# Kernel optimization log

Hardware: AMD Instinct MI355X
Metric: run time of the kernel (lower is better)

Reference implementation:

```python
import jax, jax.numpy as jnp
import numpy as np

B, T, C = 2, 2048, 2048
N_HEAD = 16
N_KV = 4
HEAD = C // N_HEAD  # 128
GROUP = N_HEAD // N_KV


def setup_inputs() -> dict:
    key = jax.random.key(0)
    ks = jax.random.split(key, 5)
    s = 1.0 / np.sqrt(C)
    return {
        "x": jax.random.normal(ks[0], (B, T, C), dtype=jnp.float32),
        "Wq": jax.random.normal(ks[1], (C, C), dtype=jnp.float32) * s,
        "Wk": jax.random.normal(ks[2], (C, N_KV * HEAD), dtype=jnp.float32) * s,
        "Wv": jax.random.normal(ks[3], (C, N_KV * HEAD), dtype=jnp.float32) * s,
        "Wo": jax.random.normal(ks[4], (C, C), dtype=jnp.float32) * s,
    }


def reference(x, Wq, Wk, Wv, Wo):
    Bx, Tx, Cx = x.shape
    q = (x @ Wq).reshape(Bx, Tx, N_HEAD, HEAD).transpose(0, 2, 1, 3)  # (B,H,T,D)
    k = (x @ Wk).reshape(Bx, Tx, N_KV, HEAD).transpose(0, 2, 1, 3)    # (B,KV,T,D)
    v = (x @ Wv).reshape(Bx, Tx, N_KV, HEAD).transpose(0, 2, 1, 3)
    # expand kv heads to query heads (GQA): repeat each kv head GROUP times
    k = jnp.repeat(k, GROUP, axis=1)  # (B,H,T,D)
    v = jnp.repeat(v, GROUP, axis=1)
    scale = 1.0 / np.sqrt(HEAD).astype(np.float32)
    att = jnp.einsum("bhqd,bhkd->bhqk", q, k) * scale  # (B,H,T,T)
    causal = jnp.tril(jnp.ones((Tx, Tx), dtype=bool))
    att = jnp.where(causal[None, None], att, -jnp.inf)
    att = jax.nn.softmax(att, axis=-1)
    y = jnp.einsum("bhqk,bhkd->bhqd", att, v)  # (B,H,T,D)
    y = y.transpose(0, 2, 1, 3).reshape(Bx, Tx, Cx)
    return y @ Wo
```

## Files before the change

kernel.cpp:

```cpp
#include <hip/hip_runtime.h>
#include <cstdint>

typedef unsigned short u16;
typedef unsigned int u32;
typedef __attribute__((ext_vector_type(8))) __bf16 bf16x8;
typedef __attribute__((ext_vector_type(4))) float f32x4;
typedef __attribute__((ext_vector_type(4))) unsigned short u16x4;

#define AS1 __attribute__((address_space(1)))
#define AS3 __attribute__((address_space(3)))

__device__ __forceinline__ void gload16(const void* g, void* l) {
    __builtin_amdgcn_global_load_lds((AS1 void*)g, (AS3 void*)l, 16, 0, 0);
}

__device__ __forceinline__ u16 f2bf(float f) {
    return __builtin_bit_cast(u16, (__bf16)f);
}

__device__ __forceinline__ void store_c(u16* p, float v)   { *p = f2bf(v); }
__device__ __forceinline__ void store_c(float* p, float v) { *p = v; }

__global__ __launch_bounds__(256) void prep(
    const float* __restrict__ x,  const float* __restrict__ Wq,
    const float* __restrict__ Wk, const float* __restrict__ Wv,
    const float* __restrict__ Wo,
    u16* __restrict__ xb, u16* __restrict__ WqkvT, u16* __restrict__ WoT)
{
    __shared__ float tile[32][33];
    const int z = blockIdx.z;
    const int tx = threadIdx.x, ty = threadIdx.y;

    if (z >= 4) {
        int gb  = (z - 4) * 4096 + blockIdx.y * 64 + blockIdx.x;
        int i   = (gb * 256 + ty * 32 + tx) * 4;
        float4 v = *(const float4*)(x + i);
        u16x4 o = { f2bf(v.x), f2bf(v.y), f2bf(v.z), f2bf(v.w) };
        *(u16x4*)(xb + i) = o;
        return;
    }

    const float* in; u16* out; int C;
    if (z == 0)      { in = Wq; out = WqkvT;                         C = 2048; }
    else if (z == 1) { in = Wk; out = WqkvT + (size_t)2048 * 2048;   C = 512;  }
    else if (z == 2) { in = Wv; out = WqkvT + (size_t)2560 * 2048;   C = 512;  }
    else             { in = Wo; out = WoT;                           C = 2048; }

    int c0 = blockIdx.x * 32, r0 = blockIdx.y * 32;
    if (c0 >= C) return;
#pragma unroll
    for (int i = 0; i < 32; i += 8)
        tile[ty + i][tx] = in[(size_t)(r0 + ty + i) * C + c0 + tx];
    __syncthreads();
#pragma unroll
    for (int i = 0; i < 32; i += 8)
        out[(size_t)(c0 + ty + i) * 2048 + r0 + tx] = f2bf(tile[tx][ty + i]);
}

__global__ void vtrans(const u16* __restrict__ QKV, u16* __restrict__ VT) {
    __shared__ u16 tile[32][33];
    int b = blockIdx.z;
    int c0 = blockIdx.x * 32, r0 = blockIdx.y * 32;
    int tx = threadIdx.x, ty = threadIdx.y;
#pragma unroll
    for (int i = 0; i < 32; i += 8)
        tile[ty + i][tx] = QKV[(size_t)(b * 2048 + r0 + ty + i) * 3072 + 2560 + c0 + tx];
    __syncthreads();
#pragma unroll
    for (int i = 0; i < 32; i += 8)
        VT[(size_t)(b * 512 + c0 + ty + i) * 2048 + r0 + tx] = tile[tx][ty + i];
}

template <typename OT>
__global__ __launch_bounds__(256, 2) void gemm_bt(
    const u16* __restrict__ A, const u16* __restrict__ Bt,
    OT* __restrict__ C, int M, int N, int K)
{
    __shared__ u16 As[128 * 64];
    __shared__ u16 Bs[128 * 64];
    const int tid  = threadIdx.x;
    const int wave = tid >> 6, lane = tid & 63;
    const int quad = lane >> 4, l15 = lane & 15;
    const int bm0 = blockIdx.y * 128, bn0 = blockIdx.x * 128;
    const int wr = (wave >> 1) * 64, wc = (wave & 1) * 64;

    const f32x4 zero = {0.f, 0.f, 0.f, 0.f};
    f32x4 acc[4][4];
#pragma unroll
    for (int i = 0; i < 4; ++i)
#pragma unroll
        for (int j = 0; j < 4; ++j) acc[i][j] = zero;

    const int srow = lane >> 3;
    const int jsw  = ((lane & 7) ^ srow) * 8;

    for (int k0 = 0; k0 < K; k0 += 64) {
#pragma unroll
        for (int i = 0; i < 4; ++i) {
            int c = wave * 4 + i;
            gload16(A  + (size_t)(bm0 + c * 8 + srow) * K + k0 + jsw, As + c * 512);
            gload16(Bt + (size_t)(bn0 + c * 8 + srow) * K + k0 + jsw, Bs + c * 512);
        }
        __syncthreads();
#pragma unroll
        for (int ks = 0; ks < 2; ++ks) {
            bf16x8 a[4], b[4];
#pragma unroll
            for (int t = 0; t < 4; ++t) {
                int rd = ((ks * 4 + quad) ^ (l15 & 7)) * 8;
                a[t] = *(const bf16x8*)(As + (wr + t * 16 + l15) * 64 + rd);
                b[t] = *(const bf16x8*)(Bs + (wc + t * 16 + l15) * 64 + rd);
            }
#pragma unroll
            for (int i = 0; i < 4; ++i)
#pragma unroll
                for (int j = 0; j < 4; ++j)
                    acc[i][j] = __builtin_amdgcn_mfma_f32_16x16x32_bf16(a[i], b[j], acc[i][j], 0, 0, 0);
        }
        __syncthreads();
    }
#pragma unroll
    for (int i = 0; i < 4; ++i) {
        int grow = bm0 + wr + i * 16 + quad * 4;
#pragma unroll
        for (int j = 0; j < 4; ++j) {
            int gcol = bn0 + wc + j * 16 + l15;
#pragma unroll
            for (int r = 0; r < 4; ++r)
                store_c(&C[(size_t)(grow + r) * N + gcol], acc[i][j][r]);
        }
    }
}

__global__ __launch_bounds__(512, 4) void attn(
    const u16* __restrict__ QKV, const u16* __restrict__ VT, u16* __restrict__ Y)
{
    __shared__ u16 Ks[2][64 * 128];
    __shared__ u16 Vs[128 * 64];
    __shared__ u16 Ps[8][16 * 72];

    const int tid  = threadIdx.x;
    const int wave = tid >> 6, lane = tid & 63;
    const int quad = lane >> 4, l15 = lane & 15;
    const int w4 = wave & 3;
    int pi = blockIdx.x;
    const int bh = blockIdx.y;
    if (bh >= 16) pi = 15 - pi;
    const int qtA = 2 * pi, qtB = 2 * pi + 1;
    const int b = bh >> 4, h = bh & 15, kv = h >> 2;

    const int myqt = (wave < 4) ? qtA : qtB;
    const int q0 = myqt * 64 + w4 * 16;

    bf16x8 aq[4];
    {
        const u16* qp = QKV + (size_t)(b * 2048 + q0 + l15) * 3072 + h * 128 + quad * 8;
#pragma unroll
        for (int ks = 0; ks < 4; ++ks) aq[ks] = *(const bf16x8*)(qp + ks * 32);
    }

    bf16x8 ones;
#pragma unroll
    for (int i = 0; i < 8; ++i) ones[i] = __builtin_bit_cast(__bf16, (u16)0x3F80);

    const f32x4 zero = {0.f, 0.f, 0.f, 0.f};
    f32x4 o[9];
#pragma unroll
    for (int i = 0; i < 9; ++i) o[i] = zero;

    const u16* Kbase = QKV + 2048 + kv * 128;
    const u16* Vbase = VT + (size_t)((b * 4 + kv) * 128) * 2048;
    u16* pw = &Ps[wave][0];

    const int kr = lane >> 4;
    const int vr = lane >> 3;
    const int vjs = ((lane & 7) ^ vr) * 8;

    auto stageK = [&](int buf, int kt) {
#pragma unroll
        for (int i = 0; i < 2; ++i) {
            int ci = wave * 2 + i;
            int krow = ci * 4 + kr;
            int kjs = ((lane & 15) ^ (krow & 15)) * 8;
            gload16(Kbase + (size_t)(b * 2048 + kt * 64 + krow) * 3072 + kjs,
                    &Ks[buf][ci * 512]);
        }
    };
    auto stageV = [&](int kt) {
#pragma unroll
        for (int i = 0; i < 2; ++i) {
            int ci = wave * 2 + i;
            int vrow = ci * 8 + vr;
            gload16(Vbase + (size_t)vrow * 2048 + kt * 64 + vjs, &Vs[ci * 512]);
        }
    };

    const float c1 = 0.12752817f;
    const float c2 = 28.85390082f;

    stageK(0, 0);
    __syncthreads();

    for (int kt = 0; kt <= qtB; ++kt) {
        const int cur = kt & 1;
        stageV(kt);
        const bool pre = (kt < qtB);
        if (pre) stageK(cur ^ 1, kt + 1);

        const bool act = (kt <= myqt);
        const u16* Ksc = &Ks[cur][0];

        if (act) {
            f32x4 s[4];
#pragma unroll
            for (int i = 0; i < 4; ++i) s[i] = zero;
            __builtin_amdgcn_s_setprio(1);
#pragma unroll
            for (int ks = 0; ks < 4; ++ks)
#pragma unroll
                for (int kc = 0; kc < 4; ++kc) {
                    bf16x8 bk = *(const bf16x8*)(Ksc + (kc * 16 + l15) * 128 + (((ks * 4 + quad) ^ l15) * 8));
                    s[kc] = __builtin_amdgcn_mfma_f32_16x16x32_bf16(aq[ks], bk, s[kc], 0, 0, 0);
                }
            __builtin_amdgcn_s_setprio(0);
            const bool diag = (kt == myqt);
#pragma unroll
            for (int kc = 0; kc < 4; ++kc)
#pragma unroll
                for (int r = 0; r < 4; ++r) {
                    float arg = fmaf(s[kc][r], c1, -c2);
                    if (diag && (kc * 16 + l15) > (w4 * 16 + quad * 4 + r)) arg = -10000.f;
                    float p = __builtin_amdgcn_exp2f(arg);
                    pw[(quad * 4 + r) * 72 + kc * 16 + l15] = f2bf(p);
                }
            asm volatile("" ::: "memory");
        }

        if (pre) asm volatile("s_waitcnt vmcnt(2)" ::: "memory");
        else     asm volatile("s_waitcnt vmcnt(0)" ::: "memory");
        __builtin_amdgcn_s_barrier();

        if (act) {
            __builtin_amdgcn_s_setprio(1);
#pragma unroll
            for (int ks2 = 0; ks2 < 2; ++ks2) {
                bf16x8 pa = *(const bf16x8*)(pw + l15 * 72 + ks2 * 32 + quad * 8);
#pragma unroll
                for (int d = 0; d < 8; ++d) {
                    bf16x8 bv = *(const bf16x8*)(Vs + (d * 16 + l15) * 64 + (((ks2 * 4 + quad) ^ (l15 & 7)) * 8));
                    o[d] = __builtin_amdgcn_mfma_f32_16x16x32_bf16(pa, bv, o[d], 0, 0, 0);
                }
                o[8] = __builtin_amdgcn_mfma_f32_16x16x32_bf16(pa, ones, o[8], 0, 0, 0);
            }
            __builtin_amdgcn_s_setprio(0);
        }

        asm volatile("s_waitcnt vmcnt(0) lgkmcnt(0)" ::: "memory");
        __builtin_amdgcn_s_barrier();
    }

    float inv[4];
#pragma unroll
    for (int r = 0; r < 4; ++r) inv[r] = 1.0f / o[8][r];
#pragma unroll
    for (int d = 0; d < 8; ++d)
#pragma unroll
        for (int r = 0; r < 4; ++r)
            Y[(size_t)(b * 2048 + q0 + quad * 4 + r) * 2048 + h * 128 + d * 16 + l15] =
                f2bf(o[d][r] * inv[r]);
}

extern "C" void kernel_launch(void* const* d_in, const int* in_sizes, int n_in,
                              void* d_out, int out_size, void* d_ws, size_t ws_size,
                              hipStream_t stream)
{
    const float* x  = (const float*)d_in[0];
    const float* Wq = (const float*)d_in[1];
    const float* Wk = (const float*)d_in[2];
    const float* Wv = (const float*)d_in[3];
    const float* Wo = (const float*)d_in[4];
    float* out = (float*)d_out;

    char* ws = (char*)d_ws;
    u16* xb    = (u16*)ws; ws += (size_t)4096 * 2048 * 2;
    u16* WqkvT = (u16*)ws; ws += (size_t)3072 * 2048 * 2;
    u16* WoT   = (u16*)ws; ws += (size_t)2048 * 2048 * 2;
    u16* QKVb  = (u16*)ws; ws += (size_t)4096 * 3072 * 2;
    u16* VT    = (u16*)ws;
    u16* Y     = xb;

    dim3 tblk(32, 8, 1);
    prep<<<dim3(64, 64, 6), tblk, 0, stream>>>(x, Wq, Wk, Wv, Wo, xb, WqkvT, WoT);

    gemm_bt<u16><<<dim3(24, 32, 1), 256, 0, stream>>>(xb, WqkvT, QKVb, 4096, 3072, 2048);

    vtrans<<<dim3(16, 64, 2), tblk, 0, stream>>>(QKVb, VT);

    attn<<<dim3(16, 32, 1), 512, 0, stream>>>(QKVb, VT, Y);

    gemm_bt<float><<<dim3(16, 32, 1), 256, 0, stream>>>(Y, WoT, out, 4096, 2048, 2048);
}
```

Measured before the change: 267.1 us.

## Split attention wave tiles 2x2 over query and key/dim halves with shared P

```diff
diff --git a/kernel.cpp b/kernel.cpp
--- a/kernel.cpp
+++ b/kernel.cpp
@@ -137,12 +137,14 @@
 {
     __shared__ u16 Ks[2][64 * 128];
     __shared__ u16 Vs[128 * 64];
-    __shared__ u16 Ps[8][16 * 72];
+    __shared__ u16 Ps[2][64 * 72];
 
     const int tid  = threadIdx.x;
     const int wave = tid >> 6, lane = tid & 63;
     const int quad = lane >> 4, l15 = lane & 15;
     const int w4 = wave & 3;
+    const int qh = w4 >> 1;
+    const int kh = w4 & 1;
     int pi = blockIdx.x;
     const int bh = blockIdx.y;
     if (bh >= 16) pi = 15 - pi;
@@ -150,13 +152,15 @@
     const int b = bh >> 4, h = bh & 15, kv = h >> 2;
 
     const int myqt = (wave < 4) ? qtA : qtB;
-    const int q0 = myqt * 64 + w4 * 16;
-
-    bf16x8 aq[4];
+
+    bf16x8 aq[2][4];
     {
-        const u16* qp = QKV + (size_t)(b * 2048 + q0 + l15) * 3072 + h * 128 + quad * 8;
-#pragma unroll
-        for (int ks = 0; ks < 4; ++ks) aq[ks] = *(const bf16x8*)(qp + ks * 32);
+        const u16* qp = QKV + (size_t)(b * 2048 + myqt * 64 + qh * 32 + l15) * 3072 + h * 128 + quad * 8;
+#pragma unroll
+        for (int qr = 0; qr < 2; ++qr)
+#pragma unroll
+            for (int ks = 0; ks < 4; ++ks)
+                aq[qr][ks] = *(const bf16x8*)(qp + (size_t)qr * 16 * 3072 + ks * 32);
     }
 
     bf16x8 ones;
@@ -164,13 +168,16 @@
     for (int i = 0; i < 8; ++i) ones[i] = __builtin_bit_cast(__bf16, (u16)0x3F80);
 
     const f32x4 zero = {0.f, 0.f, 0.f, 0.f};
-    f32x4 o[9];
-#pragma unroll
-    for (int i = 0; i < 9; ++i) o[i] = zero;
+    f32x4 o[2][4];
+#pragma unroll
+    for (int qr = 0; qr < 2; ++qr)
+#pragma unroll
+        for (int j = 0; j < 4; ++j) o[qr][j] = zero;
+    f32x4 o8[2] = {zero, zero};
 
     const u16* Kbase = QKV + 2048 + kv * 128;
     const u16* Vbase = VT + (size_t)((b * 4 + kv) * 128) * 2048;
-    u16* pw = &Ps[wave][0];
+    u16* pg = &Ps[wave >> 2][0];
 
     const int kr = lane >> 4;
     const int vr = lane >> 3;
@@ -211,46 +218,60 @@
         const u16* Ksc = &Ks[cur][0];
 
         if (act) {
-            f32x4 s[4];
-#pragma unroll
-            for (int i = 0; i < 4; ++i) s[i] = zero;
+            f32x4 s[2][2];
+#pragma unroll
+            for (int i = 0; i < 2; ++i)
+#pragma unroll
+                for (int j = 0; j < 2; ++j) s[i][j] = zero;
             __builtin_amdgcn_s_setprio(1);
 #pragma unroll
-            for (int ks = 0; ks < 4; ++ks)
-#pragma unroll
-                for (int kc = 0; kc < 4; ++kc) {
-                    bf16x8 bk = *(const bf16x8*)(Ksc + (kc * 16 + l15) * 128 + (((ks * 4 + quad) ^ l15) * 8));
-                    s[kc] = __builtin_amdgcn_mfma_f32_16x16x32_bf16(aq[ks], bk, s[kc], 0, 0, 0);
+            for (int ks = 0; ks < 4; ++ks) {
+                const int rd = ((ks * 4 + quad) ^ l15) * 8;
+                bf16x8 bk0 = *(const bf16x8*)(Ksc + (kh * 32 + l15) * 128 + rd);
+                bf16x8 bk1 = *(const bf16x8*)(Ksc + (kh * 32 + 16 + l15) * 128 + rd);
+#pragma unroll
+                for (int qr = 0; qr < 2; ++qr) {
+                    s[qr][0] = __builtin_amdgcn_mfma_f32_16x16x32_bf16(aq[qr][ks], bk0, s[qr][0], 0, 0, 0);
+                    s[qr][1] = __builtin_amdgcn_mfma_f32_16x16x32_bf16(aq[qr][ks], bk1, s[qr][1], 0, 0, 0);
                 }
+            }
             __builtin_amdgcn_s_setprio(0);
             const bool diag = (kt == myqt);
 #pragma unroll
-            for (int kc = 0; kc < 4; ++kc)
-#pragma unroll
-                for (int r = 0; r < 4; ++r) {
-                    float arg = fmaf(s[kc][r], c1, -c2);
-                    if (diag && (kc * 16 + l15) > (w4 * 16 + quad * 4 + r)) arg = -10000.f;
-                    float p = __builtin_amdgcn_exp2f(arg);
-                    pw[(quad * 4 + r) * 72 + kc * 16 + l15] = f2bf(p);
-                }
+            for (int qr = 0; qr < 2; ++qr)
+#pragma unroll
+                for (int kc = 0; kc < 2; ++kc)
+#pragma unroll
+                    for (int r = 0; r < 4; ++r) {
+                        float arg = fmaf(s[qr][kc][r], c1, -c2);
+                        int key = kh * 32 + kc * 16 + l15;
+                        int row = qh * 32 + qr * 16 + quad * 4 + r;
+                        if (diag && key > row) arg = -10000.f;
+                        float p = __builtin_amdgcn_exp2f(arg);
+                        pg[row * 72 + key] = f2bf(p);
+                    }
             asm volatile("" ::: "memory");
         }
 
-        if (pre) asm volatile("s_waitcnt vmcnt(2)" ::: "memory");
-        else     asm volatile("s_waitcnt vmcnt(0)" ::: "memory");
+        if (pre) asm volatile("s_waitcnt vmcnt(2) lgkmcnt(0)" ::: "memory");
+        else     asm volatile("s_waitcnt vmcnt(0) lgkmcnt(0)" ::: "memory");
         __builtin_amdgcn_s_barrier();
 
         if (act) {
             __builtin_amdgcn_s_setprio(1);
 #pragma unroll
             for (int ks2 = 0; ks2 < 2; ++ks2) {
-                bf16x8 pa = *(const bf16x8*)(pw + l15 * 72 + ks2 * 32 + quad * 8);
-#pragma unroll
-                for (int d = 0; d < 8; ++d) {
-                    bf16x8 bv = *(const bf16x8*)(Vs + (d * 16 + l15) * 64 + (((ks2 * 4 + quad) ^ (l15 & 7)) * 8));
-                    o[d] = __builtin_amdgcn_mfma_f32_16x16x32_bf16(pa, bv, o[d], 0, 0, 0);
+                bf16x8 pa0 = *(const bf16x8*)(pg + (qh * 32 + l15) * 72 + ks2 * 32 + quad * 8);
+                bf16x8 pa1 = *(const bf16x8*)(pg + (qh * 32 + 16 + l15) * 72 + ks2 * 32 + quad * 8);
+                const int vswz = ((ks2 * 4 + quad) ^ (l15 & 7)) * 8;
+#pragma unroll
+                for (int dj = 0; dj < 4; ++dj) {
+                    bf16x8 bv = *(const bf16x8*)(Vs + ((kh * 4 + dj) * 16 + l15) * 64 + vswz);
+                    o[0][dj] = __builtin_amdgcn_mfma_f32_16x16x32_bf16(pa0, bv, o[0][dj], 0, 0, 0);
+                    o[1][dj] = __builtin_amdgcn_mfma_f32_16x16x32_bf16(pa1, bv, o[1][dj], 0, 0, 0);
                 }
-                o[8] = __builtin_amdgcn_mfma_f32_16x16x32_bf16(pa, ones, o[8], 0, 0, 0);
+                o8[0] = __builtin_amdgcn_mfma_f32_16x16x32_bf16(pa0, ones, o8[0], 0, 0, 0);
+                o8[1] = __builtin_amdgcn_mfma_f32_16x16x32_bf16(pa1, ones, o8[1], 0, 0, 0);
             }
             __builtin_amdgcn_s_setprio(0);
         }
@@ -259,15 +280,18 @@
         __builtin_amdgcn_s_barrier();
     }
 
-    float inv[4];
-#pragma unroll
-    for (int r = 0; r < 4; ++r) inv[r] = 1.0f / o[8][r];
-#pragma unroll
-    for (int d = 0; d < 8; ++d)
-#pragma unroll
-        for (int r = 0; r < 4; ++r)
-            Y[(size_t)(b * 2048 + q0 + quad * 4 + r) * 2048 + h * 128 + d * 16 + l15] =
-                f2bf(o[d][r] * inv[r]);
+#pragma unroll
+    for (int qr = 0; qr < 2; ++qr) {
+        float inv[4];
+#pragma unroll
+        for (int r = 0; r < 4; ++r) inv[r] = 1.0f / o8[qr][r];
+#pragma unroll
+        for (int dj = 0; dj < 4; ++dj)
+#pragma unroll
+            for (int r = 0; r < 4; ++r)
+                Y[(size_t)(b * 2048 + myqt * 64 + qh * 32 + qr * 16 + quad * 4 + r) * 2048
+                  + h * 128 + (kh * 4 + dj) * 16 + l15] = f2bf(o[qr][dj][r] * inv[r]);
+    }
 }
 
 extern "C" void kernel_launch(void* const* d_in, const int* in_sizes, int n_in,
```

Measured after the change: 270.6 us. No clear change (+1.3%).

## Split attention into one q-tile per block and read V directly from global

Applied to the files above, without the earlier changes.

```diff
diff --git a/kernel.cpp b/kernel.cpp
--- a/kernel.cpp
+++ b/kernel.cpp
@@ -132,25 +132,19 @@
     }
 }
 
-__global__ __launch_bounds__(512, 4) void attn(
+__global__ __launch_bounds__(256, 3) void attn(
     const u16* __restrict__ QKV, const u16* __restrict__ VT, u16* __restrict__ Y)
 {
     __shared__ u16 Ks[2][64 * 128];
-    __shared__ u16 Vs[128 * 64];
-    __shared__ u16 Ps[8][16 * 72];
+    __shared__ u16 Ps[4][16 * 72];
 
     const int tid  = threadIdx.x;
     const int wave = tid >> 6, lane = tid & 63;
     const int quad = lane >> 4, l15 = lane & 15;
-    const int w4 = wave & 3;
-    int pi = blockIdx.x;
+    const int qt = blockIdx.x;
     const int bh = blockIdx.y;
-    if (bh >= 16) pi = 15 - pi;
-    const int qtA = 2 * pi, qtB = 2 * pi + 1;
     const int b = bh >> 4, h = bh & 15, kv = h >> 2;
-
-    const int myqt = (wave < 4) ? qtA : qtB;
-    const int q0 = myqt * 64 + w4 * 16;
+    const int q0 = qt * 64 + wave * 16;
 
     bf16x8 aq[4];
     {
@@ -173,27 +167,17 @@
     u16* pw = &Ps[wave][0];
 
     const int kr = lane >> 4;
-    const int vr = lane >> 3;
-    const int vjs = ((lane & 7) ^ vr) * 8;
 
     auto stageK = [&](int buf, int kt) {
 #pragma unroll
-        for (int i = 0; i < 2; ++i) {
-            int ci = wave * 2 + i;
+        for (int i = 0; i < 4; ++i) {
+            int ci = wave * 4 + i;
             int krow = ci * 4 + kr;
             int kjs = ((lane & 15) ^ (krow & 15)) * 8;
             gload16(Kbase + (size_t)(b * 2048 + kt * 64 + krow) * 3072 + kjs,
                     &Ks[buf][ci * 512]);
         }
     };
-    auto stageV = [&](int kt) {
-#pragma unroll
-        for (int i = 0; i < 2; ++i) {
-            int ci = wave * 2 + i;
-            int vrow = ci * 8 + vr;
-            gload16(Vbase + (size_t)vrow * 2048 + kt * 64 + vjs, &Vs[ci * 512]);
-        }
-    };
 
     const float c1 = 0.12752817f;
     const float c2 = 28.85390082f;
@@ -201,16 +185,13 @@
     stageK(0, 0);
     __syncthreads();
 
-    for (int kt = 0; kt <= qtB; ++kt) {
+    for (int kt = 0; kt <= qt; ++kt) {
         const int cur = kt & 1;
-        stageV(kt);
-        const bool pre = (kt < qtB);
-        if (pre) stageK(cur ^ 1, kt + 1);
-
-        const bool act = (kt <= myqt);
+        if (kt < qt) stageK(cur ^ 1, kt + 1);
+
         const u16* Ksc = &Ks[cur][0];
 
-        if (act) {
+        {
             f32x4 s[4];
 #pragma unroll
             for (int i = 0; i < 4; ++i) s[i] = zero;
@@ -223,31 +204,28 @@
                     s[kc] = __builtin_amdgcn_mfma_f32_16x16x32_bf16(aq[ks], bk, s[kc], 0, 0, 0);
                 }
             __builtin_amdgcn_s_setprio(0);
-            const bool diag = (kt == myqt);
+            const bool diag = (kt == qt);
 #pragma unroll
             for (int kc = 0; kc < 4; ++kc)
 #pragma unroll
                 for (int r = 0; r < 4; ++r) {
                     float arg = fmaf(s[kc][r], c1, -c2);
-                    if (diag && (kc * 16 + l15) > (w4 * 16 + quad * 4 + r)) arg = -10000.f;
+                    if (diag && (kc * 16 + l15) > (wave * 16 + quad * 4 + r)) arg = -10000.f;
                     float p = __builtin_amdgcn_exp2f(arg);
                     pw[(quad * 4 + r) * 72 + kc * 16 + l15] = f2bf(p);
                 }
             asm volatile("" ::: "memory");
         }
 
-        if (pre) asm volatile("s_waitcnt vmcnt(2)" ::: "memory");
-        else     asm volatile("s_waitcnt vmcnt(0)" ::: "memory");
-        __builtin_amdgcn_s_barrier();
-
-        if (act) {
+        {
             __builtin_amdgcn_s_setprio(1);
 #pragma unroll
             for (int ks2 = 0; ks2 < 2; ++ks2) {
                 bf16x8 pa = *(const bf16x8*)(pw + l15 * 72 + ks2 * 32 + quad * 8);
+                const u16* vp = Vbase + (size_t)l15 * 2048 + kt * 64 + (ks2 * 4 + quad) * 8;
 #pragma unroll
                 for (int d = 0; d < 8; ++d) {
-                    bf16x8 bv = *(const bf16x8*)(Vs + (d * 16 + l15) * 64 + (((ks2 * 4 + quad) ^ (l15 & 7)) * 8));
+                    bf16x8 bv = *(const bf16x8*)(vp + (size_t)d * 16 * 2048);
                     o[d] = __builtin_amdgcn_mfma_f32_16x16x32_bf16(pa, bv, o[d], 0, 0, 0);
                 }
                 o[8] = __builtin_amdgcn_mfma_f32_16x16x32_bf16(pa, ones, o[8], 0, 0, 0);
@@ -255,8 +233,7 @@
             __builtin_amdgcn_s_setprio(0);
         }
 
-        asm volatile("s_waitcnt vmcnt(0) lgkmcnt(0)" ::: "memory");
-        __builtin_amdgcn_s_barrier();
+        __syncthreads();
     }
 
     float inv[4];
@@ -296,7 +273,7 @@
 
     vtrans<<<dim3(16, 64, 2), tblk, 0, stream>>>(QKVb, VT);
 
-    attn<<<dim3(16, 32, 1), 512, 0, stream>>>(QKVb, VT, Y);
+    attn<<<dim3(32, 32, 1), 256, 0, stream>>>(QKVb, VT, Y);
 
     gemm_bt<float><<<dim3(16, 32, 1), 256, 0, stream>>>(Y, WoT, out, 4096, 2048, 2048);
 }
```

New measurement: 491.6 us. 84.0% more time.

## Double-buffer V tiles and drop mid-iteration barrier in attention loop

Applied to the files above, without the earlier changes.

```diff
diff --git a/kernel.cpp b/kernel.cpp
--- a/kernel.cpp
+++ b/kernel.cpp
@@ -135,9 +135,7 @@
 __global__ __launch_bounds__(512, 4) void attn(
     const u16* __restrict__ QKV, const u16* __restrict__ VT, u16* __restrict__ Y)
 {
-    __shared__ u16 Ks[2][64 * 128];
-    __shared__ u16 Vs[128 * 64];
-    __shared__ u16 Ps[8][16 * 72];
+    __shared__ u16 SMEM[40960];
 
     const int tid  = threadIdx.x;
     const int wave = tid >> 6, lane = tid & 63;
@@ -170,28 +168,30 @@
 
     const u16* Kbase = QKV + 2048 + kv * 128;
     const u16* Vbase = VT + (size_t)((b * 4 + kv) * 128) * 2048;
-    u16* pw = &Ps[wave][0];
+    u16* pw = SMEM + 32768 + wave * 1024;
 
     const int kr = lane >> 4;
     const int vr = lane >> 3;
     const int vjs = ((lane & 7) ^ vr) * 8;
 
     auto stageK = [&](int buf, int kt) {
+        u16* dst = SMEM + buf * 8192;
 #pragma unroll
         for (int i = 0; i < 2; ++i) {
             int ci = wave * 2 + i;
             int krow = ci * 4 + kr;
             int kjs = ((lane & 15) ^ (krow & 15)) * 8;
             gload16(Kbase + (size_t)(b * 2048 + kt * 64 + krow) * 3072 + kjs,
-                    &Ks[buf][ci * 512]);
+                    dst + ci * 512);
         }
     };
-    auto stageV = [&](int kt) {
+    auto stageV = [&](int buf, int kt) {
+        u16* dst = SMEM + 16384 + buf * 8192;
 #pragma unroll
         for (int i = 0; i < 2; ++i) {
             int ci = wave * 2 + i;
             int vrow = ci * 8 + vr;
-            gload16(Vbase + (size_t)vrow * 2048 + kt * 64 + vjs, &Vs[ci * 512]);
+            gload16(Vbase + (size_t)vrow * 2048 + kt * 64 + vjs, dst + ci * 512);
         }
     };
 
@@ -199,16 +199,19 @@
     const float c2 = 28.85390082f;
 
     stageK(0, 0);
+    stageV(0, 0);
     __syncthreads();
 
     for (int kt = 0; kt <= qtB; ++kt) {
         const int cur = kt & 1;
-        stageV(kt);
-        const bool pre = (kt < qtB);
-        if (pre) stageK(cur ^ 1, kt + 1);
+        if (kt < qtB) {
+            stageV(cur ^ 1, kt + 1);
+            stageK(cur ^ 1, kt + 1);
+        }
 
         const bool act = (kt <= myqt);
-        const u16* Ksc = &Ks[cur][0];
+        const u16* Ksc = SMEM + cur * 8192;
+        const u16* Vsc = SMEM + 16384 + cur * 8192;
 
         if (act) {
             f32x4 s[4];
@@ -231,23 +234,19 @@
                     float arg = fmaf(s[kc][r], c1, -c2);
                     if (diag && (kc * 16 + l15) > (w4 * 16 + quad * 4 + r)) arg = -10000.f;
                     float p = __builtin_amdgcn_exp2f(arg);
-                    pw[(quad * 4 + r) * 72 + kc * 16 + l15] = f2bf(p);
+                    int row = quad * 4 + r;
+                    int gsw = ((kc * 2 + (l15 >> 3)) ^ (row & 7)) * 8;
+                    pw[row * 64 + gsw + (l15 & 7)] = f2bf(p);
                 }
             asm volatile("" ::: "memory");
-        }
-
-        if (pre) asm volatile("s_waitcnt vmcnt(2)" ::: "memory");
-        else     asm volatile("s_waitcnt vmcnt(0)" ::: "memory");
-        __builtin_amdgcn_s_barrier();
-
-        if (act) {
+
             __builtin_amdgcn_s_setprio(1);
 #pragma unroll
             for (int ks2 = 0; ks2 < 2; ++ks2) {
-                bf16x8 pa = *(const bf16x8*)(pw + l15 * 72 + ks2 * 32 + quad * 8);
+                bf16x8 pa = *(const bf16x8*)(pw + l15 * 64 + (((ks2 * 4 + quad) ^ (l15 & 7)) * 8));
 #pragma unroll
                 for (int d = 0; d < 8; ++d) {
-                    bf16x8 bv = *(const bf16x8*)(Vs + (d * 16 + l15) * 64 + (((ks2 * 4 + quad) ^ (l15 & 7)) * 8));
+                    bf16x8 bv = *(const bf16x8*)(Vsc + (d * 16 + l15) * 64 + (((ks2 * 4 + quad) ^ (l15 & 7)) * 8));
                     o[d] = __builtin_amdgcn_mfma_f32_16x16x32_bf16(pa, bv, o[d], 0, 0, 0);
                 }
                 o[8] = __builtin_amdgcn_mfma_f32_16x16x32_bf16(pa, ones, o[8], 0, 0, 0);
@@ -255,8 +254,7 @@
             __builtin_amdgcn_s_setprio(0);
         }
 
-        asm volatile("s_waitcnt vmcnt(0) lgkmcnt(0)" ::: "memory");
-        __builtin_amdgcn_s_barrier();
+        __syncthreads();
     }
 
     float inv[4];
```

Result: no change. 268.7 us (+0.6%).
